# Kernel tuning notes

Hardware: AMD Instinct MI355X
Metric: run time of the kernel (lower is better)

## Reference

```python
import jax, jax.numpy as jnp
import numpy as np

DIM = 384
HEADS = 12
WS = 7     # window_size
SS = 3     # shift_size
MR = 4     # mlp_ratio
HH = 56
WW = 56
B = 16


def _layernorm(x, g, b, eps=1e-5):
    m = jnp.mean(x, axis=-1, keepdims=True)
    v = jnp.var(x, axis=-1, keepdims=True)
    return (x - m) * jax.lax.rsqrt(v + eps) * g + b


def _gen_mask(H, W, ws, ss):
    # H, W divisible by ws here, so Hp==H, Wp==W (static, numpy at trace time)
    img = np.zeros((H, W), np.float32)
    sl = [slice(0, -ws), slice(-ws, -ss), slice(-ss, None)]
    cnt = 0
    for hs in sl:
        for wsl in sl:
            img[hs, wsl] = cnt
            cnt += 1
    mw = img.reshape(H // ws, ws, W // ws, ws).transpose(0, 2, 1, 3).reshape(-1, ws * ws)
    am = mw[:, None, :] - mw[:, :, None]           # (nW, L, L)
    return jnp.asarray(np.where(am != 0, -100.0, 0.0).astype(np.float32))


def setup_inputs() -> dict:
    key = jax.random.key(0)
    ks = jax.random.split(key, 8)
    s = 0.02
    d, hd = DIM, DIM * MR
    return {
        "x": jax.random.normal(ks[0], (B, HH * WW, d), jnp.float32),
        "ln1_g": jnp.ones((d,), jnp.float32),
        "ln1_b": jnp.zeros((d,), jnp.float32),
        "qkv_w": jax.random.normal(ks[1], (d, 3 * d), jnp.float32) * s,  # qkv_bias=False
        "proj_w": jax.random.normal(ks[2], (d, d), jnp.float32) * s,
        "proj_b": jnp.zeros((d,), jnp.float32),
        "ln2_g": jnp.ones((d,), jnp.float32),
        "ln2_b": jnp.zeros((d,), jnp.float32),
        "fc1_w": jax.random.normal(ks[3], (d, hd), jnp.float32) * s,
        "fc1_b": jnp.zeros((hd,), jnp.float32),
        "dw_k": jax.random.normal(ks[4], (hd, 1, 3, 3), jnp.float32) * s,  # depthwise 3x3
        "dw_b": jnp.zeros((hd,), jnp.float32),
        "fc2_w": jax.random.normal(ks[5], (hd, d), jnp.float32) * s,
        "fc2_b": jnp.zeros((d,), jnp.float32),
        "H": HH,
        "W": WW,
    }


def reference(x, ln1_g, ln1_b, qkv_w, proj_w, proj_b, ln2_g, ln2_b,
              fc1_w, fc1_b, dw_k, dw_b, fc2_w, fc2_b, H, W):
    Bb, N, C = x.shape
    L = WS * WS
    nW = (H // WS) * (W // WS)
    hd_dim = C // HEADS
    scale = hd_dim ** (-0.5)

    # ---- windowed attention branch ----
    h = x
    xn = _layernorm(x, ln1_g, ln1_b).reshape(Bb, H, W, C)
    xs = jnp.roll(xn, (-SS, -SS), axis=(1, 2))  # shift_size > 0
    mask = _gen_mask(H, W, WS, SS)              # (nW, L, L)

    # window partition: (B*nW, L, C)
    xw = xs.reshape(Bb, H // WS, WS, W // WS, WS, C)
    xw = xw.transpose(0, 1, 3, 2, 4, 5).reshape(-1, L, C)

    qkv = xw @ qkv_w                            # (B*nW, L, 3C)
    qkv = qkv.reshape(-1, L, 3, HEADS, hd_dim).transpose(2, 0, 3, 1, 4)
    q, k, v = qkv[0], qkv[1], qkv[2]            # (B*nW, heads, L, hd)

    attn = jnp.einsum('whqd,whkd->whqk', q, k) * scale  # (B*nW, heads, L, L)
    attn = attn.reshape(Bb, nW, HEADS, L, L) + mask[None, :, None]
    attn = jax.nn.softmax(attn.reshape(-1, HEADS, L, L), axis=-1)
    out = jnp.einsum('whqk,whkd->whqd', attn, v)        # (B*nW, heads, L, hd)
    out = out.transpose(0, 2, 1, 3).reshape(-1, L, C)
    out = out @ proj_w + proj_b

    # window reverse (NOTE: original source does NOT roll back the shift)
    xr = out.reshape(Bb, H // WS, W // WS, WS, WS, C)
    xr = xr.transpose(0, 1, 3, 2, 4, 5).reshape(Bb, H, W, C)
    x = h + xr.reshape(Bb, N, C)

    # ---- DWConv MLP branch ----
    h = x
    xn = _layernorm(x, ln2_g, ln2_b)
    x1 = xn @ fc1_w + fc1_b                     # (B, N, 4C)
    hdc = x1.shape[-1]
    xc = x1.transpose(0, 2, 1).reshape(Bb, hdc, H, W)
    xc = jax.lax.conv_general_dilated(
        xc, dw_k, (1, 1), ((1, 1), (1, 1)),
        dimension_numbers=('NCHW', 'OIHW', 'NCHW'),
        feature_group_count=hdc) + dw_b[None, :, None, None]
    x1 = xc.reshape(Bb, hdc, N).transpose(0, 2, 1)
    x1 = jax.nn.gelu(x1, approximate=False)     # torch nn.GELU default = exact erf
    x1 = x1 @ fc2_w + fc2_b
    return h + x1
```

## Files before the change

kernel.cpp:

```cpp
#include <hip/hip_runtime.h>


using bf16x8 = __attribute__((ext_vector_type(8))) short;
using f32x4  = __attribute__((ext_vector_type(4))) float;
using h16x4  = __attribute__((ext_vector_type(4))) _Float16;

#define CDIM  384
#define N3C   1152
#define NHID  1536

__device__ __forceinline__ float bf2f(unsigned short u){
  union { unsigned int i; float f; } x; x.i = ((unsigned int)u) << 16; return x.f;
}
__device__ __forceinline__ unsigned short f2bf(float f){
  union { float f; unsigned int i; } x; x.f = f;
  unsigned int r = x.i + 0x7fffu + ((x.i >> 16) & 1u);
  return (unsigned short)(r >> 16);
}
__device__ __forceinline__ void gload16(const void* g, void* l){
  __builtin_amdgcn_global_load_lds(
      (const __attribute__((address_space(1))) unsigned int*)g,
      (__attribute__((address_space(3))) unsigned int*)l, 16, 0, 0);
}

__global__ __launch_bounds__(256)
void cvtT_kern(const float* __restrict__ w, unsigned short* __restrict__ wt, int K, int N){
  __shared__ unsigned short t[32][33];
  int bk = blockIdx.x, bn = blockIdx.y;
  int tr = threadIdx.x >> 5, tc = threadIdx.x & 31;
  #pragma unroll
  for (int r = tr; r < 32; r += 8)
    t[r][tc] = f2bf(w[(size_t)(bk*32 + r) * N + bn*32 + tc]);
  __syncthreads();
  #pragma unroll
  for (int r = tr; r < 32; r += 8)
    wt[(size_t)(bn*32 + r) * K + bk*32 + tc] = t[tc][r];
}

__global__ __launch_bounds__(256)
void cvtDW_kern(const float* __restrict__ k, unsigned short* __restrict__ wt){
  int i = blockIdx.x * 256 + threadIdx.x;
  if (i < NHID * 9){
    int c = i / 9, tap = i % 9;
    union { _Float16 h; unsigned short u; } cvt; cvt.h = (_Float16)k[i];
    wt[tap * NHID + c] = cvt.u;
  }
}

__global__ __launch_bounds__(64)
void ln_kern(const float* __restrict__ xin, const float* __restrict__ g,
             const float* __restrict__ bsh, unsigned short* __restrict__ out,
             int row_off, int do_shift)
{
  int blk = blockIdx.x, t = threadIdx.x;
  size_t src;
  if (do_shift){
    int gl = row_off + blk;
    int bb = gl / 3136, rem = gl % 3136;
    int wi = rem / 49, l = rem % 49;
    int h = (wi >> 3) * 7 + l / 7;
    int w = (wi & 7) * 7 + l % 7;
    int sh = h + 3; if (sh >= 56) sh -= 56;
    int sw = w + 3; if (sw >= 56) sw -= 56;
    src = ((size_t)bb * 3136 + sh * 56 + sw) * CDIM;
  } else {
    src = (size_t)blk * CDIM;
  }
  float v[6]; float s = 0.f;
  #pragma unroll
  for (int j = 0; j < 6; j++){ v[j] = xin[src + j*64 + t]; s += v[j]; }
  #pragma unroll
  for (int m = 32; m >= 1; m >>= 1) s += __shfl_xor(s, m);
  float mean = s * (1.f/384.f);
  float q = 0.f;
  #pragma unroll
  for (int j = 0; j < 6; j++){ float d = v[j] - mean; q += d * d; }
  #pragma unroll
  for (int m = 32; m >= 1; m >>= 1) q += __shfl_xor(q, m);
  float rstd = rsqrtf(q * (1.f/384.f) + 1e-5f);
  size_t dst = (size_t)blk * CDIM;
  #pragma unroll
  for (int j = 0; j < 6; j++){
    int c = j*64 + t;
    out[dst + c] = f2bf((v[j] - mean) * rstd * g[c] + bsh[c]);
  }
}

template<int MODE, int BN>
__global__ __launch_bounds__(256)
void gemm_kern(const unsigned short* __restrict__ A, int lda,
               const unsigned short* __restrict__ Bt, int K, int N,
               const float* __restrict__ bias, const float* __restrict__ resid,
               void* __restrict__ outv, int row_off)
{
  constexpr int NI = BN / 32;
  __shared__ __align__(16) unsigned short Al[2][128 * 32];
  __shared__ __align__(16) unsigned short Bl[2][BN * 32];
  int tid = threadIdx.x;
  int lane = tid & 63, wv = tid >> 6;

  int nwg = gridDim.x, bid = blockIdx.x;
  int q8 = nwg >> 3, r8 = nwg & 7;
  int xcd = bid & 7, idx = bid >> 3;
  int l = ((xcd < r8) ? xcd * (q8 + 1) : r8 * (q8 + 1) + (xcd - r8) * q8) + idx;
  const int NT = N / BN;
  int m0 = (l / NT) * 128, n0 = (l % NT) * BN;

  const int wrow = (wv >> 1) * 64;
  const int wcol = (wv & 1) * (BN / 2);
  const int lr = lane & 15, lk = (lane >> 4) * 8;

  auto STAGE = [&](int buf, int k0){
    #pragma unroll
    for (int i = 0; i < 2; i++){
      int c = i*256 + tid;
      gload16(&A[(size_t)(m0 + (c >> 2)) * lda + k0 + (c & 3) * 8],
              &Al[buf][(i*256 + wv*64) * 8]);
    }
    #pragma unroll
    for (int i = 0; i < BN/64; i++){
      int c = i*256 + tid;
      gload16(&Bt[(size_t)(n0 + (c >> 2)) * K + k0 + (c & 3) * 8],
              &Bl[buf][(i*256 + wv*64) * 8]);
    }
  };

  f32x4 acc[4][NI] = {};
  const int nt = K / 32;
  STAGE(0, 0);
  for (int t = 0; t < nt; ++t){
    int cur = t & 1;
    if (t + 1 < nt){
      STAGE(cur ^ 1, (t + 1) * 32);
      if constexpr (BN == 128) asm volatile("s_waitcnt vmcnt(4)" ::: "memory");
      else                     asm volatile("s_waitcnt vmcnt(3)" ::: "memory");
    } else {
      asm volatile("s_waitcnt vmcnt(0)" ::: "memory");
    }
    __builtin_amdgcn_s_barrier();
    __builtin_amdgcn_sched_barrier(0);
    bf16x8 af[4], bfr[NI];
    #pragma unroll
    for (int mi = 0; mi < 4; mi++) af[mi] = *(const bf16x8*)&Al[cur][(wrow + mi*16 + lr)*32 + lk];
    #pragma unroll
    for (int ni = 0; ni < NI; ni++) bfr[ni] = *(const bf16x8*)&Bl[cur][(wcol + ni*16 + lr)*32 + lk];
    #pragma unroll
    for (int mi = 0; mi < 4; mi++)
      #pragma unroll
      for (int ni = 0; ni < NI; ni++)
        acc[mi][ni] = __builtin_amdgcn_mfma_f32_16x16x32_bf16(af[mi], bfr[ni], acc[mi][ni], 0, 0, 0);
    __builtin_amdgcn_sched_barrier(0);
    __builtin_amdgcn_s_barrier();
    __builtin_amdgcn_sched_barrier(0);
  }

  #pragma unroll
  for (int mi = 0; mi < 4; mi++)
  #pragma unroll
  for (int ni = 0; ni < NI; ni++)
  #pragma unroll
  for (int j = 0; j < 4; j++){
    int row = m0 + wrow + mi*16 + (lane >> 4) * 4 + j;
    int col = n0 + wcol + ni*16 + lr;
    float val = acc[mi][ni][j];
    if (MODE == 0){
      ((unsigned short*)outv)[(size_t)row * N + col] = f2bf(val);
    } else if (MODE == 1){
      union { _Float16 h; unsigned short u; } cvt;
      cvt.h = (_Float16)(val + bias[col]);
      ((unsigned short*)outv)[(size_t)row * N + col] = cvt.u;
    } else if (MODE == 2){
      val += bias[col];
      int gl = row_off + row;
      int bb = gl / 3136, rem = gl % 3136;
      int wi = rem / 49, l2 = rem % 49;
      int n = ((wi >> 3) * 7 + l2 / 7) * 56 + (wi & 7) * 7 + l2 % 7;
      size_t idx2 = ((size_t)bb * 3136 + n) * CDIM + col;
      ((float*)outv)[idx2] = resid[idx2] + val;
    } else {
      size_t idx2 = (size_t)(row_off + row) * CDIM + col;
      ((float*)outv)[idx2] = resid[idx2] + val + bias[col];
    }
  }
}

__global__ __launch_bounds__(256)
void attn_kern(unsigned short* __restrict__ qkv)
{
  __shared__ __align__(16) unsigned short Vt[32 * 64];
  __shared__ __align__(16) unsigned short Pl[4][16 * 64];
  __shared__ unsigned char idt[49];
  int blk = blockIdx.x;
  int win = blk / 12, head = blk % 12;
  int tid = threadIdx.x;
  int wid = tid >> 6, l = tid & 63;
  int g = l >> 4, q15 = l & 15;
  size_t base = (size_t)win * 49 * N3C + (size_t)head * 32;
  const unsigned short* kp = qkv + base + 384;
  const unsigned short* vp = qkv + base + 768;

  int wi = win & 63;
  if (wid == 0 && l < 49){
    int h = (wi >> 3) * 7 + l / 7;
    int w = (wi & 7) * 7 + l % 7;
    idt[l] = (unsigned char)((h < 49 ? 0 : (h < 53 ? 1 : 2)) * 3 +
                             (w < 49 ? 0 : (w < 53 ? 1 : 2)));
  }
  {
    int c = tid;
    int key = c >> 2, keyc = min(key, 48), d0 = (c & 3) * 8;
    bf16x8 v = *(const bf16x8*)&vp[(size_t)keyc * N3C + d0];
    #pragma unroll
    for (int j = 0; j < 8; j++){
      int d = d0 + j;
      *(unsigned short*)((char*)Vt + d * 128 + ((key * 2) ^ ((d & 7) << 4))) =
          (unsigned short)v[j];
    }
  }
  __syncthreads();

  bf16x8 kf[4];
  #pragma unroll
  for (int kt = 0; kt < 4; kt++){
    int krow = min(kt * 16 + q15, 48);
    kf[kt] = *(const bf16x8*)&kp[(size_t)krow * N3C + g * 8];
  }
  bf16x8 vf[2][2];
  #pragma unroll
  for (int kb = 0; kb < 2; kb++)
    #pragma unroll
    for (int nt = 0; nt < 2; nt++){
      int n = nt * 16 + q15;
      vf[kb][nt] = *(const bf16x8*)((char*)Vt + n * 128 + ((kb * 64 + g * 16) ^ ((n & 7) << 4)));
    }
  unsigned int kidp[4];
  #pragma unroll
  for (int kt = 0; kt < 4; kt++){
    unsigned int p = 0;
    #pragma unroll
    for (int r = 0; r < 4; r++)
      p |= ((unsigned int)idt[min(kt * 16 + 4 * g + r, 48)]) << (8 * r);
    kidp[kt] = p;
  }

  const float scale = 0.17677669529663687f;
  const f32x4 zf = {0.f, 0.f, 0.f, 0.f};
  const int qt = wid;
  int qrow = min(qt * 16 + q15, 48);
  bf16x8 qf = *(const bf16x8*)&qkv[base + (size_t)qrow * N3C + g * 8];
  f32x4 s[4];
  #pragma unroll
  for (int kt = 0; kt < 4; kt++)
    s[kt] = __builtin_amdgcn_mfma_f32_16x16x32_bf16(kf[kt], qf, zf, 0, 0, 0);
  int qid = idt[qrow];
  float mx = -1e30f;
  #pragma unroll
  for (int kt = 0; kt < 4; kt++)
    #pragma unroll
    for (int r = 0; r < 4; r++){
      float x = s[kt][r] * scale;
      int idk = (kidp[kt] >> (8 * r)) & 255;
      x += (idk != qid) ? -100.f : 0.f;
      if (kt * 16 + 4 * g + r >= 49) x = -3.0e38f;
      s[kt][r] = x;
      mx = fmaxf(mx, x);
    }
  mx = fmaxf(mx, __shfl_xor(mx, 16));
  mx = fmaxf(mx, __shfl_xor(mx, 32));
  float sum = 0.f;
  #pragma unroll
  for (int kt = 0; kt < 4; kt++)
    #pragma unroll
    for (int r = 0; r < 4; r++){
      float e = __expf(s[kt][r] - mx);
      s[kt][r] = e; sum += e;
    }
  sum += __shfl_xor(sum, 16);
  sum += __shfl_xor(sum, 32);
  float inv = 1.f / sum;
  char* plc = (char*)Pl[wid];
  #pragma unroll
  for (int kt = 0; kt < 4; kt++){
    float e0 = s[kt][0] * inv, e1 = s[kt][1] * inv;
    float e2 = s[kt][2] * inv, e3 = s[kt][3] * inv;
    unsigned int pa, pb;
    asm("v_cvt_pk_bf16_f32 %0, %1, %2" : "=v"(pa) : "v"(e0), "v"(e1));
    asm("v_cvt_pk_bf16_f32 %0, %1, %2" : "=v"(pb) : "v"(e2), "v"(e3));
    uint2 w2; w2.x = pa; w2.y = pb;
    *(uint2*)(plc + q15 * 128 + ((kt * 32 + g * 8) ^ ((q15 & 7) << 4))) = w2;
  }
  asm volatile("s_waitcnt lgkmcnt(0)" ::: "memory");
  __builtin_amdgcn_sched_barrier(0);
  f32x4 o[2] = {zf, zf};
  #pragma unroll
  for (int kb = 0; kb < 2; kb++){
    bf16x8 pf = *(const bf16x8*)(plc + q15 * 128 + ((kb * 64 + g * 16) ^ ((q15 & 7) << 4)));
    #pragma unroll
    for (int nt = 0; nt < 2; nt++)
      o[nt] = __builtin_amdgcn_mfma_f32_16x16x32_bf16(pf, vf[kb][nt], o[nt], 0, 0, 0);
  }
  #pragma unroll
  for (int nt = 0; nt < 2; nt++)
    #pragma unroll
    for (int r = 0; r < 4; r++){
      int qp = qt * 16 + 4 * g + r;
      if (qp < 49)
        qkv[base + (size_t)qp * N3C + nt * 16 + q15] = f2bf(o[nt][r]);
    }
}

#define CONV_T 8
__global__ __launch_bounds__(384)
void conv_gelu_kern(const unsigned short* __restrict__ x1, const unsigned short* __restrict__ wt,
                    const float* __restrict__ kb, unsigned short* __restrict__ out)
{
  int tid = threadIdx.x;
  int c0 = tid * 4;
  h16x4 wv[9];
  #pragma unroll
  for (int j = 0; j < 9; j++) wv[j] = *(const h16x4*)&wt[j * NHID + c0];
  float4 bias = *(const float4*)&kb[c0];

  int n0 = blockIdx.x * CONV_T;
  int rem = n0 % 3136;
  int h = rem / 56, w0 = rem % 56;
  const int hm = (h > 0), hp = (h < 55);
  const unsigned short* base = x1 + (size_t)n0 * NHID + c0;
  const h16x4 z4 = {(_Float16)0, (_Float16)0, (_Float16)0, (_Float16)0};

  h16x4 win[3][3];
  if (w0 > 0){
    win[0][0] = hm ? *(const h16x4*)(base + (-56 - 1) * NHID) : z4;
    win[1][0] =      *(const h16x4*)(base - NHID);
    win[2][0] = hp ? *(const h16x4*)(base + (56 - 1) * NHID) : z4;
  } else { win[0][0] = z4; win[1][0] = z4; win[2][0] = z4; }
  win[0][1] = hm ? *(const h16x4*)(base - 56 * NHID) : z4;
  win[1][1] =      *(const h16x4*)(base);
  win[2][1] = hp ? *(const h16x4*)(base + 56 * NHID) : z4;

  #pragma unroll
  for (int t = 0; t < CONV_T; t++){
    int w = w0 + t;
    const int snew = (t + 2) % 3;
    if (w + 1 <= 55){
      const unsigned short* p = base + (t + 1) * NHID;
      win[0][snew] = hm ? *(const h16x4*)(p - 56 * NHID) : z4;
      win[1][snew] =      *(const h16x4*)(p);
      win[2][snew] = hp ? *(const h16x4*)(p + 56 * NHID) : z4;
    } else { win[0][snew] = z4; win[1][snew] = z4; win[2][snew] = z4; }
    const int s0 = t % 3, s1 = (t + 1) % 3, s2 = snew;
    h16x4 acc = win[0][s0] * wv[0];
    acc += win[0][s1] * wv[1];
    acc += win[0][s2] * wv[2];
    acc += win[1][s0] * wv[3];
    acc += win[1][s1] * wv[4];
    acc += win[1][s2] * wv[5];
    acc += win[2][s0] * wv[6];
    acc += win[2][s1] * wv[7];
    acc += win[2][s2] * wv[8];
    float v0 = (float)acc[0] + bias.x;
    float v1 = (float)acc[1] + bias.y;
    float v2 = (float)acc[2] + bias.z;
    float v3 = (float)acc[3] + bias.w;
    float g0, g1, g2, g3;
    {
      float u, tq, z, e, s;
      u = v0*v0; tq = fmaf(u, 0.07135481627f, 1.5957691216f); z = v0*tq;
      e = __expf(-z); s = __builtin_amdgcn_rcpf(1.f + e); g0 = v0 * s;
      u = v1*v1; tq = fmaf(u, 0.07135481627f, 1.5957691216f); z = v1*tq;
      e = __expf(-z); s = __builtin_amdgcn_rcpf(1.f + e); g1 = v1 * s;
      u = v2*v2; tq = fmaf(u, 0.07135481627f, 1.5957691216f); z = v2*tq;
      e = __expf(-z); s = __builtin_amdgcn_rcpf(1.f + e); g2 = v2 * s;
      u = v3*v3; tq = fmaf(u, 0.07135481627f, 1.5957691216f); z = v3*tq;
      e = __expf(-z); s = __builtin_amdgcn_rcpf(1.f + e); g3 = v3 * s;
    }
    unsigned int pa, pb;
    asm("v_cvt_pk_bf16_f32 %0, %1, %2" : "=v"(pa) : "v"(g0), "v"(g1));
    asm("v_cvt_pk_bf16_f32 %0, %1, %2" : "=v"(pb) : "v"(g2), "v"(g3));
    uint2 w2; w2.x = pa; w2.y = pb;
    *(uint2*)&out[(size_t)(n0 + t) * NHID + c0] = w2;
  }
}

extern "C" void kernel_launch(void* const* d_in, const int* in_sizes, int n_in,
                              void* d_out, int out_size, void* d_ws, size_t ws_size,
                              hipStream_t stream)
{
  const float* x      = (const float*)d_in[0];
  const float* ln1_g  = (const float*)d_in[1];
  const float* ln1_b  = (const float*)d_in[2];
  const float* qkv_w  = (const float*)d_in[3];
  const float* proj_w = (const float*)d_in[4];
  const float* proj_b = (const float*)d_in[5];
  const float* ln2_g  = (const float*)d_in[6];
  const float* ln2_b  = (const float*)d_in[7];
  const float* fc1_w  = (const float*)d_in[8];
  const float* fc1_b  = (const float*)d_in[9];
  const float* dw_k   = (const float*)d_in[10];
  const float* dw_b   = (const float*)d_in[11];
  const float* fc2_w  = (const float*)d_in[12];
  const float* fc2_b  = (const float*)d_in[13];
  float* outp = (float*)d_out;

  const size_t WS_NEED = 90270720;
  if (ws_size < WS_NEED) return;
  char* ws = (char*)d_ws;
  unsigned short* xw   = (unsigned short*)(ws);
  unsigned short* qkvh = (unsigned short*)(ws + 19267584);
  unsigned short* xn2q = (unsigned short*)(ws);
  unsigned short* x1q  = (unsigned short*)(ws + 9633792);
  unsigned short* x1gq = (unsigned short*)(ws + 48168960);
  unsigned short* wqkv = (unsigned short*)(ws + 86704128);
  unsigned short* wproj= (unsigned short*)(ws + 87588864);
  unsigned short* wfc1 = (unsigned short*)(ws + 87883776);
  unsigned short* wfc2 = (unsigned short*)(ws + 89063424);
  unsigned short* wdw  = (unsigned short*)(ws + 90243072);

  cvtT_kern<<<dim3(12, 36), 256, 0, stream>>>(qkv_w,  wqkv, 384, 1152);
  cvtT_kern<<<dim3(12, 12), 256, 0, stream>>>(proj_w, wproj, 384, 384);
  cvtT_kern<<<dim3(12, 48), 256, 0, stream>>>(fc1_w,  wfc1, 384, 1536);
  cvtT_kern<<<dim3(48, 12), 256, 0, stream>>>(fc2_w,  wfc2, 1536, 384);
  cvtDW_kern<<<(NHID*9 + 255)/256, 256, 0, stream>>>(dw_k, wdw);

  for (int hf = 0; hf < 2; hf++){
    int ro = hf * 25088;
    ln_kern<<<25088, 64, 0, stream>>>(x, ln1_g, ln1_b, xw, ro, 1);
    gemm_kern<0,128><<<196*9, 256, 0, stream>>>(xw, 384, wqkv, 384, 1152,
                                                nullptr, nullptr, qkvh, 0);
    attn_kern<<<6144, 256, 0, stream>>>(qkvh);
    gemm_kern<2,64><<<196*6, 256, 0, stream>>>(qkvh, 1152, wproj, 384, 384,
                                               proj_b, x, outp, ro);
  }

  for (int qt = 0; qt < 4; qt++){
    int ro = qt * 12544;
    ln_kern<<<12544, 64, 0, stream>>>(outp + (size_t)ro * CDIM, ln2_g, ln2_b, xn2q, 0, 0);
    gemm_kern<1,128><<<98*12, 256, 0, stream>>>(xn2q, 384, wfc1, 384, 1536,
                                                fc1_b, nullptr, x1q, 0);
    conv_gelu_kern<<<12544 / CONV_T, 384, 0, stream>>>(x1q, wdw, dw_b, x1gq);
    gemm_kern<3,64><<<98*6, 256, 0, stream>>>(x1gq, 1536, wfc2, 1536, 384,
                                              fc2_b, outp, outp, ro);
  }
}
```

Before: 605.6 us.

## Triple-buffer GEMM LDS staging and split-K the fc2 GEMM with a reduction kernel

Raises GEMM shared-memory staging from two to three buffers so two K-tiles are prefetched ahead, with adjusted vmcnt waits. It also splits the fc2 GEMM (K=1536) into two K halves, doubling the grid to 1176 blocks. Each half writes fp32 partials, and a new reduction kernel adds the partials, bias and residual. This targets low occupancy and exposed load latency in fc2, at the cost of more LDS per block, an extra partial-buffer round trip through memory, and an extra launch.

New measurement: 652.9 us. 1.08x slower.

```diff
diff --git a/kernel.cpp b/kernel.cpp
--- a/kernel.cpp
+++ b/kernel.cpp
@@ -86,16 +86,16 @@
   }
 }
 
-template<int MODE, int BN>
+template<int MODE, int BN, int KS>
 __global__ __launch_bounds__(256)
 void gemm_kern(const unsigned short* __restrict__ A, int lda,
-               const unsigned short* __restrict__ Bt, int K, int N,
+               const unsigned short* __restrict__ Bt, int K, int ldb, int N,
                const float* __restrict__ bias, const float* __restrict__ resid,
                void* __restrict__ outv, int row_off)
 {
   constexpr int NI = BN / 32;
-  __shared__ __align__(16) unsigned short Al[2][128 * 32];
-  __shared__ __align__(16) unsigned short Bl[2][BN * 32];
+  __shared__ __align__(16) unsigned short Al[3][128 * 32];
+  __shared__ __align__(16) unsigned short Bl[3][BN * 32];
   int tid = threadIdx.x;
   int lane = tid & 63, wv = tid >> 6;
 
@@ -104,7 +104,11 @@
   int xcd = bid & 7, idx = bid >> 3;
   int l = ((xcd < r8) ? xcd * (q8 + 1) : r8 * (q8 + 1) + (xcd - r8) * q8) + idx;
   const int NT = N / BN;
-  int m0 = (l / NT) * 128, n0 = (l % NT) * BN;
+  int bps = nwg / KS;
+  int ks = l / bps, l2 = l % bps;
+  int m0 = (l2 / NT) * 128, n0 = (l2 % NT) * BN;
+  const unsigned short* Ab = A + (size_t)ks * K;
+  const unsigned short* Btb = Bt + (size_t)ks * K;
 
   const int wrow = (wv >> 1) * 64;
   const int wcol = (wv & 1) * (BN / 2);
@@ -114,13 +118,13 @@
     #pragma unroll
     for (int i = 0; i < 2; i++){
       int c = i*256 + tid;
-      gload16(&A[(size_t)(m0 + (c >> 2)) * lda + k0 + (c & 3) * 8],
+      gload16(&Ab[(size_t)(m0 + (c >> 2)) * lda + k0 + (c & 3) * 8],
               &Al[buf][(i*256 + wv*64) * 8]);
     }
     #pragma unroll
     for (int i = 0; i < BN/64; i++){
       int c = i*256 + tid;
-      gload16(&Bt[(size_t)(n0 + (c >> 2)) * K + k0 + (c & 3) * 8],
+      gload16(&Btb[(size_t)(n0 + (c >> 2)) * ldb + k0 + (c & 3) * 8],
               &Bl[buf][(i*256 + wv*64) * 8]);
     }
   };
@@ -128,10 +132,14 @@
   f32x4 acc[4][NI] = {};
   const int nt = K / 32;
   STAGE(0, 0);
+  STAGE(1, 32);
   for (int t = 0; t < nt; ++t){
-    int cur = t & 1;
-    if (t + 1 < nt){
-      STAGE(cur ^ 1, (t + 1) * 32);
+    int cur = t % 3;
+    if (t + 2 < nt){
+      STAGE((t + 2) % 3, (t + 2) * 32);
+      if constexpr (BN == 128) asm volatile("s_waitcnt vmcnt(8)" ::: "memory");
+      else                     asm volatile("s_waitcnt vmcnt(6)" ::: "memory");
+    } else if (t + 1 < nt){
       if constexpr (BN == 128) asm volatile("s_waitcnt vmcnt(4)" ::: "memory");
       else                     asm volatile("s_waitcnt vmcnt(3)" ::: "memory");
     } else {
@@ -173,15 +181,34 @@
       val += bias[col];
       int gl = row_off + row;
       int bb = gl / 3136, rem = gl % 3136;
-      int wi = rem / 49, l2 = rem % 49;
-      int n = ((wi >> 3) * 7 + l2 / 7) * 56 + (wi & 7) * 7 + l2 % 7;
+      int wi = rem / 49, l3 = rem % 49;
+      int n = ((wi >> 3) * 7 + l3 / 7) * 56 + (wi & 7) * 7 + l3 % 7;
       size_t idx2 = ((size_t)bb * 3136 + n) * CDIM + col;
       ((float*)outv)[idx2] = resid[idx2] + val;
-    } else {
-      size_t idx2 = (size_t)(row_off + row) * CDIM + col;
-      ((float*)outv)[idx2] = resid[idx2] + val + bias[col];
-    }
-  }
+    } else if (MODE == 4){
+      size_t mrows = (size_t)(bps / NT) * 128;
+      ((float*)outv)[((size_t)ks * mrows + row) * N + col] = val;
+    }
+  }
+}
+
+__global__ __launch_bounds__(256)
+void fc2red_kern(const float* __restrict__ part, const float* __restrict__ resid,
+                 const float* __restrict__ bias, float* __restrict__ out, int row_off)
+{
+  int e = blockIdx.x * 256 + threadIdx.x;
+  const float4* p0 = (const float4*)part;
+  const float4* p1 = (const float4*)(part + (size_t)12544 * 384);
+  float4 a = p0[e], b = p1[e];
+  float4 bs = ((const float4*)bias)[e % 96];
+  size_t re = (size_t)row_off * 96 + e;
+  float4 r = ((const float4*)resid)[re];
+  float4 o;
+  o.x = r.x + a.x + b.x + bs.x;
+  o.y = r.y + a.y + b.y + bs.y;
+  o.z = r.z + a.z + b.z + bs.z;
+  o.w = r.w + a.w + b.w + bs.w;
+  ((float4*)out)[re] = o;
 }
 
 __global__ __launch_bounds__(256)
@@ -409,6 +436,7 @@
   unsigned short* qkvh = (unsigned short*)(ws + 19267584);
   unsigned short* xn2q = (unsigned short*)(ws);
   unsigned short* x1q  = (unsigned short*)(ws + 9633792);
+  float*          part = (float*)(ws + 9633792);
   unsigned short* x1gq = (unsigned short*)(ws + 48168960);
   unsigned short* wqkv = (unsigned short*)(ws + 86704128);
   unsigned short* wproj= (unsigned short*)(ws + 87588864);
@@ -425,20 +453,21 @@
   for (int hf = 0; hf < 2; hf++){
     int ro = hf * 25088;
     ln_kern<<<25088, 64, 0, stream>>>(x, ln1_g, ln1_b, xw, ro, 1);
-    gemm_kern<0,128><<<196*9, 256, 0, stream>>>(xw, 384, wqkv, 384, 1152,
-                                                nullptr, nullptr, qkvh, 0);
+    gemm_kern<0,128,1><<<196*9, 256, 0, stream>>>(xw, 384, wqkv, 384, 384, 1152,
+                                                  nullptr, nullptr, qkvh, 0);
     attn_kern<<<6144, 256, 0, stream>>>(qkvh);
-    gemm_kern<2,64><<<196*6, 256, 0, stream>>>(qkvh, 1152, wproj, 384, 384,
-                                               proj_b, x, outp, ro);
+    gemm_kern<2,64,1><<<196*6, 256, 0, stream>>>(qkvh, 1152, wproj, 384, 384, 384,
+                                                 proj_b, x, outp, ro);
   }
 
   for (int qt = 0; qt < 4; qt++){
     int ro = qt * 12544;
     ln_kern<<<12544, 64, 0, stream>>>(outp + (size_t)ro * CDIM, ln2_g, ln2_b, xn2q, 0, 0);
-    gemm_kern<1,128><<<98*12, 256, 0, stream>>>(xn2q, 384, wfc1, 384, 1536,
-                                                fc1_b, nullptr, x1q, 0);
+    gemm_kern<1,128,1><<<98*12, 256, 0, stream>>>(xn2q, 384, wfc1, 384, 384, 1536,
+                                                  fc1_b, nullptr, x1q, 0);
     conv_gelu_kern<<<12544 / CONV_T, 384, 0, stream>>>(x1q, wdw, dw_b, x1gq);
-    gemm_kern<3,64><<<98*6, 256, 0, stream>>>(x1gq, 1536, wfc2, 1536, 384,
-                                              fc2_b, outp, outp, ro);
-  }
-}
+    gemm_kern<4,64,2><<<98*6*2, 256, 0, stream>>>(x1gq, 1536, wfc2, 768, 1536, 384,
+                                                  nullptr, nullptr, part, 0);
+    fc2red_kern<<<4704, 256, 0, stream>>>(part, outp, fc2_b, outp, ro);
+  }
+}
```
